# Kernel optimization log

Measured on AMD Instinct MI355X. Metric: run time of the kernel, lower is better.

The kernel has to match this reference:

```python
import jax, jax.numpy as jnp
import numpy as np
from jax import lax

PAD = (3, 3)
PAD_VALUE = -1.0
POOL_SIZE = 7
POOL_STRIDE = 2


def setup_inputs() -> dict:
    key = jax.random.key(0)
    k1, k2 = jax.random.split(key)
    B, Cin, L = 64, 64, 16384
    Cout, K = 128, 7
    I = jax.random.normal(k1, (B, Cin, L), dtype=jnp.float32)
    W = jax.random.normal(k2, (Cout, Cin, K), dtype=jnp.float32)
    # Threshold params are initialized to ones in the module (requires_grad=False)
    threshold_plus = jnp.ones((Cout,), dtype=jnp.float32)
    threshold_minus = jnp.ones((Cout,), dtype=jnp.float32)
    threshold_plus_sign = jnp.ones((Cout,), dtype=jnp.float32)
    threshold_minus_sign = jnp.ones((Cout,), dtype=jnp.float32)
    return {
        "I": I,
        "W": W,
        "threshold_plus": threshold_plus,
        "threshold_minus": threshold_minus,
        "threshold_plus_sign": threshold_plus_sign,
        "threshold_minus_sign": threshold_minus_sign,
    }


def reference(I, W, threshold_plus, threshold_minus, threshold_plus_sign, threshold_minus_sign):
    # 1) ConstantPad1d(padding=(3,3), value=-1.0)
    x = jnp.pad(I, ((0, 0), (0, 0), PAD), constant_values=PAD_VALUE)
    # 2) Binarize activations and weights via sign(), then float conv1d (no bias)
    ba = jnp.sign(x)
    bw = jnp.sign(W)
    conv = lax.conv_general_dilated(
        ba, bw,
        window_strides=(1,),
        padding="VALID",
        dimension_numbers=("NCH", "OIH", "NCH"),
    )  # [B, Cout, L]
    # 3) MaxPool1d(kernel_size=7, stride=2)
    pooled = lax.reduce_window(
        conv, -jnp.inf, lax.max,
        window_dimensions=(1, 1, POOL_SIZE),
        window_strides=(1, 1, POOL_STRIDE),
        padding="VALID",
    )  # [B, Cout, Lp]
    # 4) Per-channel Threshold (vectorized over channels; 2*c > 2*t == c > t)
    tp = threshold_plus[None, :, None]
    tm = threshold_minus[None, :, None]
    ps = threshold_plus_sign[None, :, None]
    ms = threshold_minus_sign[None, :, None]
    pos_branch = jnp.where(pooled > tp, ps, -ps)
    neg_branch = jnp.where(pooled > tm, ms, -ms)
    out = jnp.where(pooled >= 0, pos_branch, neg_branch)
    return out
```

## Files before the change

### kernel.cpp

```cpp
#include <hip/hip_runtime.h>
#include <stdint.h>

#define B_    64
#define CIN   64
#define L_IN  16384
#define COUT  128
#define K_    7
#define LPAD  3
#define LPA   16416
#define LOUT  8189
#define OB    120
#define NXB   69
#define XROWS 264
#define CSTR  260

typedef int v4i __attribute__((ext_vector_type(4)));

__global__ __launch_bounds__(256) void pack_A(const float* __restrict__ I,
                                              uint64_t* __restrict__ A) {
    int b     = blockIdx.x >> 4;
    int chunk = blockIdx.x & 15;
    int t     = threadIdx.x;
    int l0    = chunk * 1024 + t * 4;
    const uint32_t* Ib = (const uint32_t*)(I + (size_t)b * CIN * L_IN + l0);
    uint32_t lo0 = 0, lo1 = 0, lo2 = 0, lo3 = 0;
    uint32_t hi0 = 0, hi1 = 0, hi2 = 0, hi3 = 0;
#pragma unroll 8
    for (int ci = 0; ci < 32; ++ci) {
        uint4 v = *(const uint4*)(Ib + (size_t)ci * L_IN);
        lo0 |= (v.x >> 31) << ci;
        lo1 |= (v.y >> 31) << ci;
        lo2 |= (v.z >> 31) << ci;
        lo3 |= (v.w >> 31) << ci;
    }
#pragma unroll 8
    for (int ci = 0; ci < 32; ++ci) {
        uint4 v = *(const uint4*)(Ib + (size_t)(ci + 32) * L_IN);
        hi0 |= (v.x >> 31) << ci;
        hi1 |= (v.y >> 31) << ci;
        hi2 |= (v.z >> 31) << ci;
        hi3 |= (v.w >> 31) << ci;
    }
    uint64_t* Ab = A + (size_t)b * LPA + (LPAD + l0);
    Ab[0] = ((uint64_t)hi0 << 32) | lo0;
    Ab[1] = ((uint64_t)hi1 << 32) | lo1;
    Ab[2] = ((uint64_t)hi2 << 32) | lo2;
    Ab[3] = ((uint64_t)hi3 << 32) | lo3;
    if (chunk == 0 && t < 6) {
        int l = (t < 3) ? t : (L_IN + t);
        A[(size_t)b * LPA + l] = ~0ULL;
    }
}

__global__ __launch_bounds__(256) void pack_Wi8(const float* __restrict__ W,
                                                uint8_t* __restrict__ Wp) {
    int idx = blockIdx.x * 256 + threadIdx.x;
    if (idx >= COUT * K_) return;
    int k  = idx >> 7;
    int co = idx & 127;
    uint8_t* dst = Wp + ((size_t)k * COUT + co) * 64;
    uint32_t d[16];
#pragma unroll
    for (int ci4 = 0; ci4 < 16; ++ci4) {
        uint32_t dw = 0;
#pragma unroll
        for (int j = 0; j < 4; ++j) {
            int ci = ci4 * 4 + j;
            uint32_t s = __float_as_uint(W[(size_t)co * CIN * K_ + ci * K_ + k]) >> 31;
            dw |= (s ? 0xFFu : 0x01u) << (8 * j);
        }
        d[ci4] = dw;
    }
#pragma unroll
    for (int q = 0; q < 4; ++q)
        *(uint4*)(dst + q * 16) = make_uint4(d[4*q+0], d[4*q+1], d[4*q+2], d[4*q+3]);
}

__global__ __launch_bounds__(256) void mfma_conv_pool(
    const uint64_t* __restrict__ A, const uint8_t* __restrict__ Wp,
    const float* __restrict__ tp_, const float* __restrict__ tm_,
    const float* __restrict__ ps_, const float* __restrict__ ms_,
    float* __restrict__ out)
{
    __shared__ __align__(16) uint8_t xs[XROWS * 64];
    __shared__ __align__(8)  int16_t cs[64 * CSTR];

    const int bx = blockIdx.x, cy = blockIdx.y, b = blockIdx.z;
    const int t = threadIdx.x;
    const int lane = t & 63, w = t >> 6;
    const int l15 = lane & 15, l4 = lane >> 4;
    const int o0 = bx * OB;
    const int c0 = 2 * o0;
    const int cout0 = cy * 64;

    const uint16_t* ap = (const uint16_t*)(A + (size_t)b * LPA);
#pragma unroll
    for (int it = 0; it < 5; ++it) {
        int idx = it * 256 + t;
        if (idx < XROWS * 4) {
            int p = idx >> 2, g = idx & 3;
            int pg = c0 + p;
            if (pg < LPA) {
                uint32_t v = ap[(size_t)pg * 4 + g];
                uint32_t dd[4];
#pragma unroll
                for (int ni = 0; ni < 4; ++ni) {
                    uint32_t n  = (v >> (4 * ni)) & 0xFu;
                    uint32_t tb = (n & 1u) | ((n & 2u) << 7) | ((n & 4u) << 14) | ((n & 8u) << 21);
                    dd[ni] = 0x01010101u ^ (tb * 0xFEu);
                }
                int gran = g ^ ((p >> 1) & 3);
                *(uint4*)(xs + p * 64 + gran * 16) = make_uint4(dd[0], dd[1], dd[2], dd[3]);
            }
        }
    }

    v4i wf[4][7];
#pragma unroll
    for (int ct = 0; ct < 4; ++ct)
#pragma unroll
        for (int k = 0; k < K_; ++k)
            wf[ct][k] = *(const v4i*)(Wp + (((size_t)k * COUT + cout0 + ct * 16 + l15) * 64 + l4 * 16));

    __syncthreads();

#pragma unroll
    for (int j = 0; j < 4; ++j) {
        const int ctile = w * 4 + j;
        v4i af[K_];
#pragma unroll
        for (int k = 0; k < K_; ++k) {
            int pl   = ctile * 16 + l15 + k;
            int gran = l4 ^ ((pl >> 1) & 3);
            af[k] = *(const v4i*)(xs + pl * 64 + gran * 16);
        }
        v4i ac0 = {0,0,0,0}, ac1 = {0,0,0,0}, ac2 = {0,0,0,0}, ac3 = {0,0,0,0};
#pragma unroll
        for (int k = 0; k < K_; ++k) {
            ac0 = __builtin_amdgcn_mfma_i32_16x16x64_i8(af[k], wf[0][k], ac0, 0, 0, 0);
            ac1 = __builtin_amdgcn_mfma_i32_16x16x64_i8(af[k], wf[1][k], ac1, 0, 0, 0);
            ac2 = __builtin_amdgcn_mfma_i32_16x16x64_i8(af[k], wf[2][k], ac2, 0, 0, 0);
            ac3 = __builtin_amdgcn_mfma_i32_16x16x64_i8(af[k], wf[3][k], ac3, 0, 0, 0);
        }
        const int crow = ctile * 16 + l4 * 4;
        {
            uint32_t p0, p1;
            int16_t* dst;
#define STORE_CT(ac, CT) \
            p0 = ((uint32_t)(ac)[0] & 0xFFFFu) | ((uint32_t)(ac)[1] << 16); \
            p1 = ((uint32_t)(ac)[2] & 0xFFFFu) | ((uint32_t)(ac)[3] << 16); \
            dst = cs + (size_t)((CT) * 16 + l15) * CSTR + crow; \
            *(uint2*)dst = make_uint2(p0, p1);
            STORE_CT(ac0, 0) STORE_CT(ac1, 1) STORE_CT(ac2, 2) STORE_CT(ac3, 3)
#undef STORE_CT
        }
    }
    __syncthreads();

#pragma unroll 1
    for (int ci = 0; ci < 16; ++ci) {
        const int cl = w * 16 + ci;
        const int co = cout0 + cl;
        const int Tip = (int)floorf(tp_[co]) + 1;
        const int Tim = (int)floorf(tm_[co]) + 1;
        const float ps = ps_[co], ms = ms_[co];
        const uint32_t* row = (const uint32_t*)(cs + (size_t)cl * CSTR);
        float* op = out + ((size_t)(b * COUT + co)) * LOUT + o0;
#pragma unroll
        for (int oi = 0; oi < 2; ++oi) {
            int o = oi * 64 + lane;
            if (o < OB && o0 + o < LOUT) {
                uint32_t d0 = row[o], d1 = row[o+1], d2 = row[o+2], d3 = row[o+3];
                int a0 = (int)(short)(d0 & 0xFFFFu), a1 = ((int)d0) >> 16;
                int a2 = (int)(short)(d1 & 0xFFFFu), a3 = ((int)d1) >> 16;
                int a4 = (int)(short)(d2 & 0xFFFFu), a5 = ((int)d2) >> 16;
                int a6 = (int)(short)(d3 & 0xFFFFu);
                int m = max(max(max(a0, a1), max(a2, a3)), max(max(a4, a5), a6));
                float r = (m >= 0) ? (m >= Tip ? ps : -ps) : (m >= Tim ? ms : -ms);
                op[o] = r;
            }
        }
    }
}

extern "C" void kernel_launch(void* const* d_in, const int* in_sizes, int n_in,
                              void* d_out, int out_size, void* d_ws, size_t ws_size,
                              hipStream_t stream) {
    const float* I  = (const float*)d_in[0];
    const float* W  = (const float*)d_in[1];
    const float* tp = (const float*)d_in[2];
    const float* tm = (const float*)d_in[3];
    const float* ps = (const float*)d_in[4];
    const float* ms = (const float*)d_in[5];
    float* out = (float*)d_out;

    uint64_t* A  = (uint64_t*)d_ws;
    uint8_t*  Wp = (uint8_t*)((char*)d_ws + (size_t)B_ * LPA * sizeof(uint64_t));

    hipLaunchKernelGGL(pack_A, dim3(B_ * 16), dim3(256), 0, stream, I, A);
    hipLaunchKernelGGL(pack_Wi8, dim3((COUT * K_ + 255) / 256), dim3(256), 0, stream, W, Wp);
    hipLaunchKernelGGL(mfma_conv_pool, dim3(NXB, 2, B_), dim3(256), 0, stream,
                       A, Wp, tp, tm, ps, ms, out);
}
```

Before: 644.5 us.

## Drop LDS input staging; load and expand activation bits directly from global per MFMA

The conv kernel no longer stages the expanded int8 activation tile in shared memory. Each wave now reads packed sign bits straight from global memory and expands them to int8 in registers, using a multiply-based bit spread, just before the MFMAs. Weights are reloaded per tap instead of held as a 28-register array, and the tile is split into two halves to cut register pressure. With launch bounds raised to 5 blocks and a smaller tile, the goal is higher occupancy and no LDS-fill barrier. The cost is redundant global and L2 reads of both activations and weights, and a margin in the workspace to cover out-of-range reads at the tail.

```diff
diff --git a/kernel.cpp b/kernel.cpp
--- a/kernel.cpp
+++ b/kernel.cpp
@@ -8,11 +8,11 @@
 #define K_    7
 #define LPAD  3
 #define LPA   16416
+#define AMARGIN 512
 #define LOUT  8189
-#define OB    120
-#define NXB   69
-#define XROWS 264
-#define CSTR  260
+#define OB    112
+#define NXB   74
+#define CSTR  236
 
 typedef int v4i __attribute__((ext_vector_type(4)));
 
@@ -76,14 +76,13 @@
         *(uint4*)(dst + q * 16) = make_uint4(d[4*q+0], d[4*q+1], d[4*q+2], d[4*q+3]);
 }
 
-__global__ __launch_bounds__(256) void mfma_conv_pool(
+__global__ __launch_bounds__(256, 5) void mfma_conv_pool(
     const uint64_t* __restrict__ A, const uint8_t* __restrict__ Wp,
     const float* __restrict__ tp_, const float* __restrict__ tm_,
     const float* __restrict__ ps_, const float* __restrict__ ms_,
     float* __restrict__ out)
 {
-    __shared__ __align__(16) uint8_t xs[XROWS * 64];
-    __shared__ __align__(8)  int16_t cs[64 * CSTR];
+    __shared__ __align__(16) int16_t cs[64 * CSTR];
 
     const int bx = blockIdx.x, cy = blockIdx.y, b = blockIdx.z;
     const int t = threadIdx.x;
@@ -94,65 +93,58 @@
     const int cout0 = cy * 64;
 
     const uint16_t* ap = (const uint16_t*)(A + (size_t)b * LPA);
+
+#pragma unroll 1
+    for (int half = 0; half < 2; ++half) {
+        const int jt0 = w * 4 + half * 2;
+        v4i ac[2][4];
 #pragma unroll
-    for (int it = 0; it < 5; ++it) {
-        int idx = it * 256 + t;
-        if (idx < XROWS * 4) {
-            int p = idx >> 2, g = idx & 3;
-            int pg = c0 + p;
-            if (pg < LPA) {
-                uint32_t v = ap[(size_t)pg * 4 + g];
-                uint32_t dd[4];
+        for (int j = 0; j < 2; ++j)
 #pragma unroll
-                for (int ni = 0; ni < 4; ++ni) {
-                    uint32_t n  = (v >> (4 * ni)) & 0xFu;
-                    uint32_t tb = (n & 1u) | ((n & 2u) << 7) | ((n & 4u) << 14) | ((n & 8u) << 21);
-                    dd[ni] = 0x01010101u ^ (tb * 0xFEu);
+            for (int c = 0; c < 4; ++c) ac[j][c] = (v4i){0, 0, 0, 0};
+
+#pragma unroll
+        for (int k = 0; k < K_; ++k) {
+            v4i wfk[4];
+#pragma unroll
+            for (int ct = 0; ct < 4; ++ct)
+                wfk[ct] = *(const v4i*)(Wp + (((size_t)k * COUT + cout0 + ct * 16 + l15) << 6) + (l4 << 4));
+
+            v4i af[2];
+#pragma unroll
+            for (int j = 0; j < 2; ++j) {
+                const int pg = c0 + (jt0 + j) * 16 + l15 + k;
+                const uint32_t h = ap[pg * 4 + l4];
+                v4i f;
+#pragma unroll
+                for (int d = 0; d < 4; ++d) {
+                    uint32_t n  = (h >> (4 * d)) & 0xFu;
+                    uint32_t tb = (n * 0x00204081u) & 0x01010101u;
+                    f[d] = (int)(0x01010101u ^ ((tb << 8) - (tb << 1)));
                 }
-                int gran = g ^ ((p >> 1) & 3);
-                *(uint4*)(xs + p * 64 + gran * 16) = make_uint4(dd[0], dd[1], dd[2], dd[3]);
+                af[j] = f;
+            }
+
+#pragma unroll
+            for (int j = 0; j < 2; ++j) {
+                ac[j][0] = __builtin_amdgcn_mfma_i32_16x16x64_i8(af[j], wfk[0], ac[j][0], 0, 0, 0);
+                ac[j][1] = __builtin_amdgcn_mfma_i32_16x16x64_i8(af[j], wfk[1], ac[j][1], 0, 0, 0);
+                ac[j][2] = __builtin_amdgcn_mfma_i32_16x16x64_i8(af[j], wfk[2], ac[j][2], 0, 0, 0);
+                ac[j][3] = __builtin_amdgcn_mfma_i32_16x16x64_i8(af[j], wfk[3], ac[j][3], 0, 0, 0);
             }
         }
-    }
-
-    v4i wf[4][7];
-#pragma unroll
-    for (int ct = 0; ct < 4; ++ct)
-#pragma unroll
-        for (int k = 0; k < K_; ++k)
-            wf[ct][k] = *(const v4i*)(Wp + (((size_t)k * COUT + cout0 + ct * 16 + l15) * 64 + l4 * 16));
-
-    __syncthreads();
 
 #pragma unroll
-    for (int j = 0; j < 4; ++j) {
-        const int ctile = w * 4 + j;
-        v4i af[K_];
+        for (int j = 0; j < 2; ++j) {
+            const int crow = (jt0 + j) * 16 + l4 * 4;
+            if (crow <= CSTR - 4) {
 #pragma unroll
-        for (int k = 0; k < K_; ++k) {
-            int pl   = ctile * 16 + l15 + k;
-            int gran = l4 ^ ((pl >> 1) & 3);
-            af[k] = *(const v4i*)(xs + pl * 64 + gran * 16);
-        }
-        v4i ac0 = {0,0,0,0}, ac1 = {0,0,0,0}, ac2 = {0,0,0,0}, ac3 = {0,0,0,0};
-#pragma unroll
-        for (int k = 0; k < K_; ++k) {
-            ac0 = __builtin_amdgcn_mfma_i32_16x16x64_i8(af[k], wf[0][k], ac0, 0, 0, 0);
-            ac1 = __builtin_amdgcn_mfma_i32_16x16x64_i8(af[k], wf[1][k], ac1, 0, 0, 0);
-            ac2 = __builtin_amdgcn_mfma_i32_16x16x64_i8(af[k], wf[2][k], ac2, 0, 0, 0);
-            ac3 = __builtin_amdgcn_mfma_i32_16x16x64_i8(af[k], wf[3][k], ac3, 0, 0, 0);
-        }
-        const int crow = ctile * 16 + l4 * 4;
-        {
-            uint32_t p0, p1;
-            int16_t* dst;
-#define STORE_CT(ac, CT) \
-            p0 = ((uint32_t)(ac)[0] & 0xFFFFu) | ((uint32_t)(ac)[1] << 16); \
-            p1 = ((uint32_t)(ac)[2] & 0xFFFFu) | ((uint32_t)(ac)[3] << 16); \
-            dst = cs + (size_t)((CT) * 16 + l15) * CSTR + crow; \
-            *(uint2*)dst = make_uint2(p0, p1);
-            STORE_CT(ac0, 0) STORE_CT(ac1, 1) STORE_CT(ac2, 2) STORE_CT(ac3, 3)
-#undef STORE_CT
+                for (int ct = 0; ct < 4; ++ct) {
+                    uint32_t p0 = ((uint32_t)ac[j][ct][0] & 0xFFFFu) | ((uint32_t)ac[j][ct][1] << 16);
+                    uint32_t p1 = ((uint32_t)ac[j][ct][2] & 0xFFFFu) | ((uint32_t)ac[j][ct][3] << 16);
+                    *(uint2*)(cs + (size_t)(ct * 16 + l15) * CSTR + crow) = make_uint2(p0, p1);
+                }
+            }
         }
     }
     __syncthreads();
@@ -163,21 +155,20 @@
         const int co = cout0 + cl;
         const int Tip = (int)floorf(tp_[co]) + 1;
         const int Tim = (int)floorf(tm_[co]) + 1;
-        const float ps = ps_[co], ms = ms_[co];
+        const float psv = ps_[co], msv = ms_[co];
         const uint32_t* row = (const uint32_t*)(cs + (size_t)cl * CSTR);
         float* op = out + ((size_t)(b * COUT + co)) * LOUT + o0;
 #pragma unroll
         for (int oi = 0; oi < 2; ++oi) {
-            int o = oi * 64 + lane;
+            const int o = oi * 64 + lane;
             if (o < OB && o0 + o < LOUT) {
-                uint32_t d0 = row[o], d1 = row[o+1], d2 = row[o+2], d3 = row[o+3];
+                uint32_t d0 = row[o], d1 = row[o + 1], d2 = row[o + 2], d3 = row[o + 3];
                 int a0 = (int)(short)(d0 & 0xFFFFu), a1 = ((int)d0) >> 16;
                 int a2 = (int)(short)(d1 & 0xFFFFu), a3 = ((int)d1) >> 16;
                 int a4 = (int)(short)(d2 & 0xFFFFu), a5 = ((int)d2) >> 16;
                 int a6 = (int)(short)(d3 & 0xFFFFu);
                 int m = max(max(max(a0, a1), max(a2, a3)), max(max(a4, a5), a6));
-                float r = (m >= 0) ? (m >= Tip ? ps : -ps) : (m >= Tim ? ms : -ms);
-                op[o] = r;
+                op[o] = (m >= 0) ? (m >= Tip ? psv : -psv) : (m >= Tim ? msv : -msv);
             }
         }
     }
@@ -195,7 +186,7 @@
     float* out = (float*)d_out;
 
     uint64_t* A  = (uint64_t*)d_ws;
-    uint8_t*  Wp = (uint8_t*)((char*)d_ws + (size_t)B_ * LPA * sizeof(uint64_t));
+    uint8_t*  Wp = (uint8_t*)((char*)d_ws + ((size_t)B_ * LPA + AMARGIN) * sizeof(uint64_t));
 
     hipLaunchKernelGGL(pack_A, dim3(B_ * 16), dim3(256), 0, stream, I, A);
     hipLaunchKernelGGL(pack_Wi8, dim3((COUT * K_ + 255) / 256), dim3(256), 0, stream, W, Wp);
```

Result: slower. 892.0 us (+38.4%).
